# Performance work log

Measured on AMD Instinct MI355X. Metric: run time of the kernel, lower is better.

Reference implementation:

```python
import jax, jax.numpy as jnp
import numpy as np

K = 3; STRIDE = 1; PAD = 1
IN_C = 256; OUT_C = 512
M = 5; TABLE_SIZE = 16
D = K * K * IN_C  # 2304


def _P(v, m):
    # ALSH preprocessing transform: append norm powers ||v||^2, ||v||^4, ...
    n2 = jnp.sum(v * v)
    powers = jnp.stack([n2 ** (2 ** i) for i in range(m)])
    return jnp.concatenate([v, powers])


def _Q(v, m):
    # ALSH query transform: append m halves
    return jnp.concatenate([v, jnp.full((m,), 0.5, v.dtype)])


def _hash_index(a, v):
    # hf followed by fmod(table_size).abs() as in the torch module
    h = jnp.floor(jnp.dot(a, v))
    return jnp.abs(jnp.mod(h, TABLE_SIZE)).astype(jnp.int32)


def _im2col(x):
    # x: (N, C, H, W) -> (K*K*C, N*h2*w2), rows ordered (kh, kw, c) to match
    # the (out, k, k, in) kernel flattening of the original module.
    N, C, H, W = x.shape
    h2 = (H - K + 2 * PAD) // STRIDE + 1
    w2 = (W - K + 2 * PAD) // STRIDE + 1
    xp = jnp.pad(x, ((0, 0), (0, 0), (PAD, PAD), (PAD, PAD)))
    cols = []
    for i in range(K):          # small fixed loop (k*k = 9)
        for j in range(K):
            cols.append(xp[:, :, i:i + h2 * STRIDE:STRIDE, j:j + w2 * STRIDE:STRIDE])
    p = jnp.stack(cols, 0)                 # (K*K, N, C, h2, w2)
    p = p.transpose(0, 2, 1, 3, 4)         # (K*K, C, N, h2, w2)
    return p.reshape(K * K * C, N * h2 * w2), h2, w2


def setup_inputs() -> dict:
    key = jax.random.key(0)
    k1, k2, k3, k4 = jax.random.split(key, 4)
    stdv = 1.0 / np.sqrt(IN_C * K * K)
    x = jax.random.normal(k1, (16, IN_C, 56, 56), dtype=jnp.float32)
    kernels = jax.random.uniform(k2, (OUT_C, D), dtype=jnp.float32,
                                 minval=-stdv, maxval=stdv)
    bias = jax.random.uniform(k3, (1, OUT_C, 1, 1), dtype=jnp.float32,
                              minval=-stdv, maxval=stdv)
    a = jax.random.normal(k4, (D + M,), dtype=jnp.float32)
    return {"x": x, "kernels": kernels, "bias": bias, "a": a, "mode": 0}


def reference(x, kernels, bias, a, mode):
    N = x.shape[0]
    patch_matr, h2, w2 = _im2col(x)  # (D, N*h2*w2)

    # --- build ALSH table: hash index per kernel row (non-differentiable) ---
    kernel_idx = jax.lax.stop_gradient(
        jax.vmap(lambda kr: _hash_index(a, _P(kr, M)))(kernels))  # (OUT_C,)

    # --- query: max over each patch row, normalized to unit vector ---
    max_row = patch_matr.max(axis=1)                    # (D,)
    unit = max_row / jnp.linalg.norm(max_row)
    q_idx = jax.lax.stop_gradient(_hash_index(a, _Q(unit, M)))

    # --- routed subset matmul, expressed as a row mask (jit-safe) ---
    mask = (kernel_idx == q_idx)                        # (OUT_C,) bool
    count = mask.sum()
    full = kernels @ patch_matr                         # (OUT_C, N*h2*w2)
    scale = jnp.where(count > 0, count / OUT_C, 1.0).astype(full.dtype)
    out = jnp.where(count > 0,
                    jnp.where(mask[:, None], full, 0.0) / scale,
                    full)

    out = out.reshape(OUT_C, N, h2 * w2).transpose(1, 0, 2)
    out = out.reshape(N, OUT_C, h2, w2)
    return out + bias
```

## Files before the change

### kernel.cpp

```cpp
#include <hip/hip_runtime.h>
#include <math.h>

#define IN_C   256
#define OUT_C  512
#define HW     3136
#define W_     56
#define D_     2304
#define TBL    16


#define XB_OFF 2375680ULL
#define XB_ROW 1856
#define P_OFF  7483392

typedef __attribute__((ext_vector_type(8))) __bf16 bf16x8;
typedef __attribute__((ext_vector_type(4))) float f32x4;

__device__ __forceinline__ ushort f2bf(float f) {
  uint b = __float_as_uint(f);
  b = b + 0x7FFFu + ((b >> 16) & 1u);
  return (ushort)(b >> 16);
}


__global__ __launch_bounds__(256) void k_setup(const float* __restrict__ x,
                                               const float* __restrict__ kern,
                                               const float* __restrict__ a,
                                               float* __restrict__ ws) {
  __shared__ __align__(16) float smem[64 * 57];
  int bx = blockIdx.x, t = threadIdx.x;

  if (bx < 3712) {
    int c0i = bx & 3;
    int n = (bx >> 2) & 15;
    int yp = bx >> 6;
    int c0 = c0i * 64, cgbase = c0i * 2;
    ushort* xb = (ushort*)((char*)ws + XB_OFF);
    const size_t CGS = (size_t)16 * 58 * XB_ROW;
    size_t rb0 = (size_t)(n * 58 + yp) * XB_ROW;
    uint4 z4 = make_uint4(0u, 0u, 0u, 0u);

    if (yp == 0 || yp == 57) {
      for (int e = t; e < 464; e += 256) {
        int cg_l = e / 232, k = e - cg_l * 232;
        *(uint4*)&xb[rb0 + (size_t)(cgbase + cg_l) * CGS + (size_t)k * 8] = z4;
      }
      return;
    }
    if (t < 16) {
      int cg_l = t >> 3, r = t & 7;
      int wp = (r >> 2) ? 57 : 0, oct = r & 3;
      *(uint4*)&xb[rb0 + (size_t)(cgbase + cg_l) * CGS + wp * 32 + oct * 8] = z4;
    }
    int y = yp - 1;
    float* Lf = smem;
    for (int e = t; e < 3584; e += 256) {
      int ci = e / 56, w = e - ci * 56;
      Lf[ci * 57 + w] = x[(size_t)(n * 256 + c0 + ci) * 3136 + y * 56 + w];
    }
    __syncthreads();
    for (int e = t; e < 448; e += 256) {
      int w = e >> 3, cg_l = (e >> 2) & 1, oct = e & 3;
      int cb = cg_l * 32 + oct * 8;
      uint pk[4];
#pragma unroll
      for (int k = 0; k < 4; k++) {
        uint lo = f2bf(Lf[(cb + 2 * k) * 57 + w]);
        uint hi = f2bf(Lf[(cb + 2 * k + 1) * 57 + w]);
        pk[k] = lo | (hi << 16);
      }
      *(uint4*)&xb[rb0 + (size_t)(cgbase + cg_l) * CGS + (w + 1) * 32 + oct * 8] =
          make_uint4(pk[0], pk[1], pk[2], pk[3]);
    }
  } else if (bx < 4736) {
    int idx = bx - 3712;
    int c = idx & 255, part = idx >> 8;
    float m[3][3];
#pragma unroll
    for (int i = 0; i < 3; i++)
#pragma unroll
      for (int j = 0; j < 3; j++) m[i][j] = -INFINITY;
    for (int e = t; e < 4 * HW; e += 256) {
      int nl = e / HW;
      int rem = e - nl * HW;
      int r = rem / W_;
      int s = rem - r * W_;
      float v = x[(size_t)((part * 4 + nl) * IN_C + c) * HW + rem];
      bool rc[3] = { r <= 54, true, r >= 1 };
      bool sc[3] = { s <= 54, true, s >= 1 };
#pragma unroll
      for (int i = 0; i < 3; i++)
#pragma unroll
        for (int j = 0; j < 3; j++)
          if (rc[i] && sc[j]) m[i][j] = fmaxf(m[i][j], v);
    }
#pragma unroll
    for (int i = 0; i < 3; i++)
#pragma unroll
      for (int j = 0; j < 3; j++)
        for (int o = 32; o; o >>= 1)
          m[i][j] = fmaxf(m[i][j], __shfl_down(m[i][j], o, 64));
    float* red = smem;
    int lane = t & 63, wid = t >> 6;
    if (lane == 0) {
#pragma unroll
      for (int i = 0; i < 3; i++)
#pragma unroll
        for (int j = 0; j < 3; j++) red[wid * 9 + i * 3 + j] = m[i][j];
    }
    __syncthreads();
    if (t < 9) {
      float v = fmaxf(fmaxf(red[0 * 9 + t], red[1 * 9 + t]),
                      fmaxf(red[2 * 9 + t], red[3 * 9 + t]));
      ws[P_OFF + (size_t)part * 2304 + (size_t)t * IN_C + c] = v;
    }
  } else if (bx < 5248) {
    int o = bx - 4736;
    const float* kr = kern + (size_t)o * D_;
    double sd = 0, sn = 0;
    for (int d = t; d < D_; d += 256) {
      double w = (double)kr[d];
      sd += (double)a[d] * w;
      sn += w * w;
    }
    double* sh = (double*)smem;
    double* sh2 = sh + 8;
    int lane = t & 63, wid = t >> 6;
    for (int off = 32; off; off >>= 1) {
      sd += __shfl_down(sd, off, 64);
      sn += __shfl_down(sn, off, 64);
    }
    if (lane == 0) { sh[wid] = sd; sh2[wid] = sn; }
    __syncthreads();
    if (t == 0) {
      double td = 0, tn = 0;
      for (int w = 0; w < 4; w++) { td += sh[w]; tn += sh2[w]; }
      double p1 = tn, p2 = p1 * p1, p4 = p2 * p2, p8 = p4 * p4, p16 = p8 * p8;
      td += (double)a[D_] * p1 + (double)a[D_ + 1] * p2 + (double)a[D_ + 2] * p4 +
            (double)a[D_ + 3] * p8 + (double)a[D_ + 4] * p16;
      long long h = (long long)floor(td);
      ((int*)ws)[2304 + o] = (int)((h % TBL + TBL) % TBL);
    }
  } else {
    int s = bx - 5248;
    uint* Wc = (uint*)((char*)ws + 16384);
    const float* src = kern + (size_t)s * D_;
    for (int e = t; e < 1152; e += 256) {
      uint lo = f2bf(src[2 * e]);
      uint hi = f2bf(src[2 * e + 1]);
      Wc[(size_t)s * 1152 + e] = lo | (hi << 16);
    }
  }
}

__global__ __launch_bounds__(512) void k_route(const float* __restrict__ a,
                                               float* __restrict__ ws) {
  int t = threadIdx.x;
  const float* P = ws + P_OFF;
  __shared__ double sh[8], sh2[8];
  __shared__ int shq, c1, c2;
  double sd = 0.0, sq = 0.0;
  if (t < 256) {
    for (int d = t; d < D_; d += 256) {
      float v = fmaxf(fmaxf(P[d], P[2304 + d]), fmaxf(P[4608 + d], P[6912 + d]));
      if ((d >> 8) != 4) v = fmaxf(v, 0.0f);
      double dv = (double)v;
      sd += (double)a[d] * dv;
      sq += dv * dv;
    }
    for (int o = 32; o; o >>= 1) {
      sd += __shfl_down(sd, o, 64);
      sq += __shfl_down(sq, o, 64);
    }
    if ((t & 63) == 0) { sh[t >> 6] = sd; sh2[t >> 6] = sq; }
  }
  __syncthreads();
  if (t == 0) {
    double td = 0, tq = 0;
    for (int w = 0; w < 4; w++) { td += sh[w]; tq += sh2[w]; }
    double dot = td / sqrt(tq);
    dot += 0.5 * ((double)a[D_] + (double)a[D_ + 1] + (double)a[D_ + 2] +
                  (double)a[D_ + 3] + (double)a[D_ + 4]);
    long long h = (long long)floor(dot);
    int q = (int)((h % TBL + TBL) % TBL);
    ((int*)ws)[2816] = q;
    shq = q;
    c1 = 0; c2 = 0;
  }
  __syncthreads();
  int* hashk = (int*)ws + 2304;
  int* cntp = (int*)ws + 2817;
  float* scalep = ws + 2818;
  int* active = (int*)ws + 2819;
  int* inact = (int*)ws + 3331;
  int q = shq;
  bool m = (hashk[t] == q);
  if (m) active[atomicAdd(&c1, 1)] = t;
  else   inact[atomicAdd(&c2, 1)] = t;
  __syncthreads();
  int c = c1;
  if (c == 0) active[t] = t;
  if (t == 0) {
    if (c > 0) { *cntp = c; *scalep = 512.0f / (float)c; }
    else       { *cntp = 512; *scalep = 1.0f; }
  }
}

#define XSTR 40
#define XSTRIDE 40
#define ASTRIDE 104

__global__ __launch_bounds__(256, 2) void k_convx(const float* __restrict__ bias,
                                                  const float* __restrict__ ws,
                                                  float* __restrict__ out) {
  const int* iws = (const int*)ws;
  int cnt = iws[2817];
  int octile = blockIdx.y;
  int rt = blockIdx.x;
  int n = blockIdx.z;
  int t = threadIdx.x;

  {
    int base = octile * 128;
    int lo = base < cnt ? cnt : base;
    int hi = base + 128;
    if (lo < hi) {
      const int* inact = iws + 3331;
      size_t nbase = (size_t)n * OUT_C * HW;
      int nin = hi - lo;
      for (int e = t; e < nin * 56; e += 256) {
        int j = e / 56, f = e - j * 56;
        int oc = inact[lo - cnt + j];
        float bv = bias[oc];
        ((float4*)out)[(nbase + (size_t)oc * HW + rt * 224) / 4 + f] =
            make_float4(bv, bv, bv, bv);
      }
    }
    if (base >= cnt) return;
  }

  float sc = ws[2818];
  const int* active = iws + 2819;
  const char* Wcb = (const char*)ws + 16384;
  const ushort* xb = (const ushort*)((const char*)ws + XB_OFF);

  int lane = t & 63, wid = t >> 6;
  int quad = lane >> 4, l16 = lane & 15;
  int ochalf = wid & 1, pxhalf = wid >> 1;

  __shared__ __align__(16) ushort X_lds[2][348 * XSTR];

  int pbase[7];
#pragma unroll
  for (int b = 0; b < 7; b++) {
    int pxl = pxhalf * 112 + b * 16 + l16;
    int rl = pxl / 56;
    int col = pxl - rl * 56;
    pbase[b] = ((rl + 1) * 58 + (col + 1)) * XSTR;
  }

  uint woff[4];
#pragma unroll
  for (int a = 0; a < 4; a++) {
    int slot = octile * 128 + ochalf * 64 + a * 16 + l16;
    int aoc = (slot < cnt) ? active[slot] : 0;
    woff[a] = (uint)aoc * 4608u + (uint)quad * 16u;
  }

  const size_t CGS = (size_t)16 * 58 * XB_ROW;
  const ushort* xsrc = xb + (size_t)(n * 58 + rt * 4) * XB_ROW;

  f32x4 acc[4][7];
#pragma unroll
  for (int a = 0; a < 4; a++)
#pragma unroll
    for (int b = 0; b < 7; b++) acc[a][b] = (f32x4){0.f, 0.f, 0.f, 0.f};

  uint4 curA[4], nA[4];
  uint4 xh; int xhj = 0; bool xhv = false;

  {
#pragma unroll
    for (int a = 0; a < 4; a++)
      curA[a] = *(const uint4*)(Wcb + woff[a]);
    for (int j = t; j < 1392; j += 256)
      *(uint4*)&X_lds[0][(j >> 2) * XSTR + (j & 3) * 8] =
          *(const uint4*)(xsrc + (size_t)j * 8);
  }
  __syncthreads();

  for (int cc = 0; cc < 8; ++cc) {
    const int xc = cc & 1;
#pragma unroll
    for (int tap = 0; tap < 9; ++tap) {
      const int tapn = (tap + 1) % 9;
      const int ccn = cc + (tap + 1) / 9;
      const bool havenext = !(cc == 7 && tap == 8);
      if (havenext) {
        uint go = (uint)(tapn * 512) + (uint)ccn * 64u;
#pragma unroll
        for (int a = 0; a < 4; a++)
          nA[a] = *(const uint4*)(Wcb + woff[a] + go);
      }
      const bool xpf = (tap < 6) && (cc < 7) && (t < 232);
      uint4 xv; int xj = tap * 232 + t;
      if (xpf)
        xv = *(const uint4*)(xsrc + (size_t)(cc + 1) * CGS + (size_t)xj * 8);

      const int kh = tap / 3, kw = tap - kh * 3;
      const int poff = ((kh - 1) * 58 + (kw - 1)) * XSTR + quad * 8;
      __builtin_amdgcn_s_setprio(1);
#pragma unroll
      for (int b = 0; b < 7; b++) {
        union { uint4 u; bf16x8 v; } cv;
        cv.u = *(const uint4*)&X_lds[xc][pbase[b] + poff];
        bf16x8 xf = cv.v;
#pragma unroll
        for (int a = 0; a < 4; a++) {
          union { uint4 u; bf16x8 v; } av;
          av.u = curA[a];
          acc[a][b] = __builtin_amdgcn_mfma_f32_16x16x32_bf16(av.v, xf,
                                                              acc[a][b], 0, 0, 0);
        }
      }
      __builtin_amdgcn_s_setprio(0);

      if (xhv)
        *(uint4*)&X_lds[xc ^ 1][(xhj >> 2) * XSTR + (xhj & 3) * 8] = xh;
      xh = xv; xhj = xj; xhv = xpf;
      if (havenext) {
#pragma unroll
        for (int a = 0; a < 4; a++) curA[a] = nA[a];
      }
    }
    __syncthreads();
  }

  size_t nbase = (size_t)n * OUT_C * HW;
#pragma unroll
  for (int a = 0; a < 4; a++) {
#pragma unroll
    for (int r = 0; r < 4; r++) {
      int slot = octile * 128 + ochalf * 64 + a * 16 + quad * 4 + r;
      if (slot < cnt) {
        int oc = active[slot];
        float bv = bias[oc];
        size_t obase = nbase + (size_t)oc * HW + rt * 224 + pxhalf * 112 + l16;
#pragma unroll
        for (int b = 0; b < 7; b++)
          out[obase + b * 16] = acc[a][b][r] * sc + bv;
      }
    }
  }
}


__global__ __launch_bounds__(256) void k_chanmax(const float* __restrict__ x,
                                                 float* __restrict__ ws) {
  int c = blockIdx.x, t = threadIdx.x;
  float m[3][3];
#pragma unroll
  for (int i = 0; i < 3; i++)
#pragma unroll
    for (int j = 0; j < 3; j++) m[i][j] = -INFINITY;
  for (int e = t; e < 16 * HW; e += 256) {
    int n = e / HW;
    int rem = e - n * HW;
    int r = rem / W_;
    int s = rem - r * W_;
    float v = x[(size_t)(n * IN_C + c) * HW + rem];
    bool rc[3] = { r <= 54, true, r >= 1 };
    bool sc[3] = { s <= 54, true, s >= 1 };
#pragma unroll
    for (int i = 0; i < 3; i++)
#pragma unroll
      for (int j = 0; j < 3; j++)
        if (rc[i] && sc[j]) m[i][j] = fmaxf(m[i][j], v);
  }
#pragma unroll
  for (int i = 0; i < 3; i++)
#pragma unroll
    for (int j = 0; j < 3; j++)
      for (int o = 32; o; o >>= 1)
        m[i][j] = fmaxf(m[i][j], __shfl_down(m[i][j], o, 64));
  __shared__ float red[4][9];
  int lane = t & 63, wid = t >> 6;
  if (lane == 0) {
#pragma unroll
    for (int i = 0; i < 3; i++)
#pragma unroll
      for (int j = 0; j < 3; j++) red[wid][i * 3 + j] = m[i][j];
  }
  __syncthreads();
  if (t < 9) {
    float v = fmaxf(fmaxf(red[0][t], red[1][t]), fmaxf(red[2][t], red[3][t]));
    int i = t / 3, j = t - i * 3;
    if (i != 1 || j != 1) v = fmaxf(v, 0.0f);
    ws[(size_t)t * IN_C + c] = v;
  }
}

__global__ __launch_bounds__(256) void k_qhash(const float* __restrict__ a,
                                               float* __restrict__ ws) {
  const float* max_row = ws;
  int t = threadIdx.x;
  double sd = 0.0, sq = 0.0;
  for (int d = t; d < D_; d += 256) {
    double v = (double)max_row[d];
    sd += (double)a[d] * v;
    sq += v * v;
  }
  __shared__ double sh[8], sh2[8];
  int lane = t & 63, wid = t >> 6;
  for (int o = 32; o; o >>= 1) {
    sd += __shfl_down(sd, o, 64);
    sq += __shfl_down(sq, o, 64);
  }
  if (lane == 0) { sh[wid] = sd; sh2[wid] = sq; }
  __syncthreads();
  if (t == 0) {
    double td = 0, tq = 0;
    for (int w = 0; w < 4; w++) { td += sh[w]; tq += sh2[w]; }
    double dot = td / sqrt(tq);
    dot += 0.5 * ((double)a[D_] + (double)a[D_ + 1] + (double)a[D_ + 2] +
                  (double)a[D_ + 3] + (double)a[D_ + 4]);
    long long h = (long long)floor(dot);
    ((int*)ws)[2816] = (int)((h % TBL + TBL) % TBL);
  }
}

__global__ __launch_bounds__(256) void k_khash(const float* __restrict__ kern,
                                               const float* __restrict__ a,
                                               float* __restrict__ ws) {
  int o = blockIdx.x, t = threadIdx.x;
  const float* kr = kern + (size_t)o * D_;
  double sd = 0, sn = 0;
  for (int d = t; d < D_; d += 256) {
    double w = (double)kr[d];
    sd += (double)a[d] * w;
    sn += w * w;
  }
  __shared__ double sh[8], sh2[8];
  int lane = t & 63, wid = t >> 6;
  for (int off = 32; off; off >>= 1) {
    sd += __shfl_down(sd, off, 64);
    sn += __shfl_down(sn, off, 64);
  }
  if (lane == 0) { sh[wid] = sd; sh2[wid] = sn; }
  __syncthreads();
  if (t == 0) {
    double td = 0, tn = 0;
    for (int w = 0; w < 4; w++) { td += sh[w]; tn += sh2[w]; }
    double p1 = tn, p2 = p1 * p1, p4 = p2 * p2, p8 = p4 * p4, p16 = p8 * p8;
    td += (double)a[D_] * p1 + (double)a[D_ + 1] * p2 + (double)a[D_ + 2] * p4 +
          (double)a[D_ + 3] * p8 + (double)a[D_ + 4] * p16;
    long long h = (long long)floor(td);
    ((int*)ws)[2304 + o] = (int)((h % TBL + TBL) % TBL);
  }
}

__global__ __launch_bounds__(512) void k_select(float* __restrict__ ws) {
  int t = threadIdx.x;
  int* hashk = (int*)ws + 2304;
  int* qidx = (int*)ws + 2816;
  int* cntp = (int*)ws + 2817;
  float* scalep = ws + 2818;
  int* active = (int*)ws + 2819;
  int* flags = (int*)ws + 3331;
  __shared__ int cnt;
  if (t == 0) cnt = 0;
  active[t] = 0;
  __syncthreads();
  int q = *qidx;
  bool m = (hashk[t] == q);
  if (m) {
    int p = atomicAdd(&cnt, 1);
    active[p] = t;
  }
  __syncthreads();
  int c = cnt;
  flags[t] = (c == 0) ? 1 : (m ? 1 : 0);
  if (c == 0) active[t] = t;
  if (t == 0) {
    if (c > 0) { *cntp = c; *scalep = 512.0f / (float)c; }
    else       { *cntp = 512; *scalep = 1.0f; }
  }
}

__global__ __launch_bounds__(256) void k_prep(const float* __restrict__ kern,
                                              float* __restrict__ ws) {
  const int* iws = (const int*)ws;
  int cnt = iws[2817];
  const int* active = iws + 2819;
  ushort* Wc = (ushort*)((char*)ws + 16384);
  int s = blockIdx.x, t = threadIdx.x;
  if (s < cnt) {
    int oc = active[s];
    const float* src = kern + (size_t)oc * D_;
    for (int e = t; e < D_; e += 256) Wc[(size_t)s * D_ + e] = f2bf(src[e]);
  } else {
    for (int e = t; e < D_; e += 256) Wc[(size_t)s * D_ + e] = 0;
  }
}

__global__ __launch_bounds__(256) void k_biasfill(const float* __restrict__ bias,
                                                  const float* __restrict__ ws,
                                                  float* __restrict__ out) {
  const int* flags = (const int*)ws + 3331;
  const int total4 = 16 * OUT_C * HW / 4;
  int stride = gridDim.x * blockDim.x;
  for (int i = blockIdx.x * blockDim.x + threadIdx.x; i < total4; i += stride) {
    int o = (i / 784) & (OUT_C - 1);
    if (!flags[o]) {
      float b = bias[o];
      ((float4*)out)[i] = make_float4(b, b, b, b);
    }
  }
}

__global__ __launch_bounds__(256, 2) void k_conv(const float* __restrict__ x,
                                                 const float* __restrict__ bias,
                                                 const float* __restrict__ ws,
                                                 float* __restrict__ out) {
  const int* iws = (const int*)ws;
  int cnt = iws[2817];
  int octile = blockIdx.y;
  if (octile * 128 >= cnt) return;
  float sc = ws[2818];
  const int* active = iws + 2819;
  const ushort* Wc = (const ushort*)((const char*)ws + 16384);
  int rt = blockIdx.x;
  int n = blockIdx.z;
  int t = threadIdx.x;
  int lane = t & 63, wid = t >> 6;
  int quad = lane >> 4, l16 = lane & 15;
  int ochalf = wid & 1, pxhalf = wid >> 1;
  __shared__ __align__(16) ushort X_lds[348 * XSTRIDE];
  __shared__ __align__(16) ushort A_lds[128 * ASTRIDE];
  const float* xin = x + (size_t)n * IN_C * HW;
  int pbase[7];
#pragma unroll
  for (int b = 0; b < 7; b++) {
    int pxl = pxhalf * 112 + b * 16 + l16;
    int rl = pxl / 56;
    int col = pxl - rl * 56;
    pbase[b] = ((rl + 1) * 58 + (col + 1)) * XSTRIDE;
  }
  f32x4 acc[4][7];
#pragma unroll
  for (int a = 0; a < 4; a++)
#pragma unroll
    for (int b = 0; b < 7; b++) acc[a][b] = (f32x4){0.f, 0.f, 0.f, 0.f};
  for (int cc = 0; cc < 8; ++cc) {
    int c0 = cc * 32;
    __syncthreads();
    for (int e = t; e < 1392; e += 256) {
      int q = e / 348;
      int p = e - q * 348;
      int rl = p / 58;
      int cp = p - rl * 58;
      int y = rt * 4 - 1 + rl;
      int xx = cp - 1;
      float vv[8];
      if ((unsigned)y < 56u && (unsigned)xx < 56u) {
        const float* src = xin + (size_t)(c0 + q * 8) * HW + y * W_ + xx;
#pragma unroll
        for (int k = 0; k < 8; k++) vv[k] = src[(size_t)k * HW];
      } else {
#pragma unroll
        for (int k = 0; k < 8; k++) vv[k] = 0.f;
      }
      uint4 pk;
      pk.x = (uint)f2bf(vv[0]) | ((uint)f2bf(vv[1]) << 16);
      pk.y = (uint)f2bf(vv[2]) | ((uint)f2bf(vv[3]) << 16);
      pk.z = (uint)f2bf(vv[4]) | ((uint)f2bf(vv[5]) << 16);
      pk.w = (uint)f2bf(vv[6]) | ((uint)f2bf(vv[7]) << 16);
      *(uint4*)&X_lds[p * XSTRIDE + q * 8] = pk;
    }
    for (int kh = 0; kh < 3; ++kh) {
      __syncthreads();
      for (int e = t; e < 1536; e += 256) {
        int oc = e / 12;
        int seg = e - oc * 12;
        int tl = seg >> 2, q = seg & 3;
        uint4 v = *(const uint4*)(Wc + (size_t)(octile * 128 + oc) * D_ +
                                  (kh * 3 + tl) * IN_C + c0 + q * 8);
        *(uint4*)&A_lds[oc * ASTRIDE + tl * 32 + q * 8] = v;
      }
      __syncthreads();
      int di = kh - 1;
#pragma unroll
      for (int djj = 0; djj < 3; ++djj) {
        int poff = (di * 58 + (djj - 1)) * XSTRIDE + quad * 8;
        bf16x8 bfr[7];
#pragma unroll
        for (int b = 0; b < 7; b++) {
          union { uint4 u; bf16x8 v; } cv;
          cv.u = *(const uint4*)&X_lds[pbase[b] + poff];
          bfr[b] = cv.v;
        }
#pragma unroll
        for (int a = 0; a < 4; a++) {
          union { uint4 u; bf16x8 v; } cv;
          cv.u = *(const uint4*)&A_lds[(ochalf * 64 + a * 16 + l16) * ASTRIDE +
                                       djj * 32 + quad * 8];
          bf16x8 af = cv.v;
#pragma unroll
          for (int b = 0; b < 7; b++)
            acc[a][b] = __builtin_amdgcn_mfma_f32_16x16x32_bf16(af, bfr[b],
                                                                acc[a][b], 0, 0, 0);
        }
      }
    }
  }
  size_t nbase = (size_t)n * OUT_C * HW;
#pragma unroll
  for (int a = 0; a < 4; a++) {
#pragma unroll
    for (int r = 0; r < 4; r++) {
      int slot = octile * 128 + ochalf * 64 + a * 16 + quad * 4 + r;
      if (slot < cnt) {
        int oc = active[slot];
        float bv = bias[oc];
        size_t obase = nbase + (size_t)oc * HW + rt * 224 + pxhalf * 112 + l16;
#pragma unroll
        for (int b = 0; b < 7; b++)
          out[obase + b * 16] = acc[a][b][r] * sc + bv;
      }
    }
  }
}

extern "C" void kernel_launch(void* const* d_in, const int* in_sizes, int n_in,
                              void* d_out, int out_size, void* d_ws, size_t ws_size,
                              hipStream_t stream) {
  const float* x    = (const float*)d_in[0];
  const float* kern = (const float*)d_in[1];
  const float* bias = (const float*)d_in[2];
  const float* a    = (const float*)d_in[3];
  float* out = (float*)d_out;
  float* ws  = (float*)d_ws;

  const size_t need = 29933568ULL + 4 * 2304 * 4;

  if (ws_size >= need) {
    k_setup<<<dim3(5760), dim3(256), 0, stream>>>(x, kern, a, ws);
    k_route<<<dim3(1), dim3(512), 0, stream>>>(a, ws);
    k_convx<<<dim3(14, 4, 16), dim3(256), 0, stream>>>(bias, ws, out);
  } else {
    k_chanmax<<<dim3(IN_C), dim3(256), 0, stream>>>(x, ws);
    k_qhash<<<dim3(1), dim3(256), 0, stream>>>(a, ws);
    k_khash<<<dim3(OUT_C), dim3(256), 0, stream>>>(kern, a, ws);
    k_select<<<dim3(1), dim3(512), 0, stream>>>(ws);
    k_prep<<<dim3(OUT_C), dim3(256), 0, stream>>>(kern, ws);
    k_biasfill<<<dim3(4096), dim3(256), 0, stream>>>(bias, ws, out);
    k_conv<<<dim3(14, 4, 16), dim3(256), 0, stream>>>(x, bias, ws, out);
  }
}
```

Baseline: 340.1 us.

## Enlarge conv tile to 128 channels by 448 pixels and stage weights in LDS

The implicit-GEMM conv block now covers 8 image rows (448 pixels) instead of 4, and each wave computes all 128 output channels over 112 pixels with 8x7 accumulators. Weights are staged through a double-buffered LDS tile shared by all waves instead of being loaded per wave into registers. This halves the grid and raises reuse of both the activation halo and the weights. The cost is doubled accumulator registers (occupancy hint lowered to 1), a larger LDS footprint, and a block barrier after every tap instead of once per channel group.

```diff
diff --git a/kernel.cpp b/kernel.cpp
--- a/kernel.cpp
+++ b/kernel.cpp
@@ -210,7 +210,7 @@
 #define XSTRIDE 40
 #define ASTRIDE 104
 
-__global__ __launch_bounds__(256, 2) void k_convx(const float* __restrict__ bias,
+__global__ __launch_bounds__(256, 1) void k_convx(const float* __restrict__ bias,
                                                   const float* __restrict__ ws,
                                                   float* __restrict__ out) {
   const int* iws = (const int*)ws;
@@ -228,11 +228,11 @@
       const int* inact = iws + 3331;
       size_t nbase = (size_t)n * OUT_C * HW;
       int nin = hi - lo;
-      for (int e = t; e < nin * 56; e += 256) {
-        int j = e / 56, f = e - j * 56;
+      for (int e = t; e < nin * 112; e += 256) {
+        int j = e / 112, f = e - j * 112;
         int oc = inact[lo - cnt + j];
         float bv = bias[oc];
-        ((float4*)out)[(nbase + (size_t)oc * HW + rt * 224) / 4 + f] =
+        ((float4*)out)[(nbase + (size_t)oc * HW) / 4 + rt * 112 + f] =
             make_float4(bv, bv, bv, bv);
       }
     }
@@ -246,44 +246,46 @@
 
   int lane = t & 63, wid = t >> 6;
   int quad = lane >> 4, l16 = lane & 15;
-  int ochalf = wid & 1, pxhalf = wid >> 1;
-
-  __shared__ __align__(16) ushort X_lds[2][348 * XSTR];
+
+  __shared__ __align__(16) ushort X_lds[2][580 * XSTR];
+  __shared__ __align__(16) ushort A_lds[2][128 * XSTR];
 
   int pbase[7];
 #pragma unroll
   for (int b = 0; b < 7; b++) {
-    int pxl = pxhalf * 112 + b * 16 + l16;
+    int pxl = wid * 112 + b * 16 + l16;
     int rl = pxl / 56;
     int col = pxl - rl * 56;
     pbase[b] = ((rl + 1) * 58 + (col + 1)) * XSTR;
   }
 
-  uint woff[4];
-#pragma unroll
-  for (int a = 0; a < 4; a++) {
-    int slot = octile * 128 + ochalf * 64 + a * 16 + l16;
-    int aoc = (slot < cnt) ? active[slot] : 0;
-    woff[a] = (uint)aoc * 4608u + (uint)quad * 16u;
-  }
+  int r0 = t >> 2;
+  int slot0 = octile * 128 + r0;
+  int slot1 = slot0 + 64;
+  int aoc0 = (slot0 < cnt) ? active[slot0] : 0;
+  int aoc1 = (slot1 < cnt) ? active[slot1] : 0;
+  const char* Wr0 = Wcb + (size_t)aoc0 * 4608 + (t & 3) * 16;
+  const char* Wr1 = Wcb + (size_t)aoc1 * 4608 + (t & 3) * 16;
+  int aoff0 = r0 * XSTR + (t & 3) * 8;
+  int aoff1 = (r0 + 64) * XSTR + (t & 3) * 8;
 
   const size_t CGS = (size_t)16 * 58 * XB_ROW;
-  const ushort* xsrc = xb + (size_t)(n * 58 + rt * 4) * XB_ROW;
-
-  f32x4 acc[4][7];
-#pragma unroll
-  for (int a = 0; a < 4; a++)
+  const ushort* xsrc = xb + (size_t)(n * 58 + rt * 8) * XB_ROW;
+
+  f32x4 acc[8][7];
+#pragma unroll
+  for (int a = 0; a < 8; a++)
 #pragma unroll
     for (int b = 0; b < 7; b++) acc[a][b] = (f32x4){0.f, 0.f, 0.f, 0.f};
 
-  uint4 curA[4], nA[4];
-  uint4 xh; int xhj = 0; bool xhv = false;
+  uint4 xh0 = {}, xh1 = {};
 
   {
-#pragma unroll
-    for (int a = 0; a < 4; a++)
-      curA[a] = *(const uint4*)(Wcb + woff[a]);
-    for (int j = t; j < 1392; j += 256)
+    uint4 a0 = *(const uint4*)Wr0;
+    uint4 a1 = *(const uint4*)Wr1;
+    *(uint4*)&A_lds[0][aoff0] = a0;
+    *(uint4*)&A_lds[0][aoff1] = a1;
+    for (int j = t; j < 2320; j += 256)
       *(uint4*)&X_lds[0][(j >> 2) * XSTR + (j & 3) * 8] =
           *(const uint4*)(xsrc + (size_t)j * 8);
   }
@@ -293,59 +295,75 @@
     const int xc = cc & 1;
 #pragma unroll
     for (int tap = 0; tap < 9; ++tap) {
+      const int cur = (cc + tap) & 1;
       const int tapn = (tap + 1) % 9;
       const int ccn = cc + (tap + 1) / 9;
       const bool havenext = !(cc == 7 && tap == 8);
+      uint4 na0, na1;
       if (havenext) {
-        uint go = (uint)(tapn * 512) + (uint)ccn * 64u;
-#pragma unroll
-        for (int a = 0; a < 4; a++)
-          nA[a] = *(const uint4*)(Wcb + woff[a] + go);
-      }
-      const bool xpf = (tap < 6) && (cc < 7) && (t < 232);
-      uint4 xv; int xj = tap * 232 + t;
-      if (xpf)
-        xv = *(const uint4*)(xsrc + (size_t)(cc + 1) * CGS + (size_t)xj * 8);
+        int off = tapn * 512 + ccn * 64;
+        na0 = *(const uint4*)(Wr0 + off);
+        na1 = *(const uint4*)(Wr1 + off);
+      }
+      const bool xi = (tap < 8) && (cc < 7);
+      uint4 xv0, xv1;
+      if (xi) {
+        int xj = tap * 290 + t;
+        xv0 = *(const uint4*)(xsrc + (size_t)(cc + 1) * CGS + (size_t)xj * 8);
+        if (t < 34)
+          xv1 = *(const uint4*)(xsrc + (size_t)(cc + 1) * CGS +
+                                (size_t)(xj + 256) * 8);
+      }
 
       const int kh = tap / 3, kw = tap - kh * 3;
       const int poff = ((kh - 1) * 58 + (kw - 1)) * XSTR + quad * 8;
-      __builtin_amdgcn_s_setprio(1);
+      bf16x8 xf[7];
 #pragma unroll
       for (int b = 0; b < 7; b++) {
         union { uint4 u; bf16x8 v; } cv;
         cv.u = *(const uint4*)&X_lds[xc][pbase[b] + poff];
-        bf16x8 xf = cv.v;
-#pragma unroll
-        for (int a = 0; a < 4; a++) {
-          union { uint4 u; bf16x8 v; } av;
-          av.u = curA[a];
-          acc[a][b] = __builtin_amdgcn_mfma_f32_16x16x32_bf16(av.v, xf,
+        xf[b] = cv.v;
+      }
+      __builtin_amdgcn_s_setprio(1);
+#pragma unroll
+      for (int a = 0; a < 8; a++) {
+        union { uint4 u; bf16x8 v; } av;
+        av.u = *(const uint4*)&A_lds[cur][(a * 16 + l16) * XSTR + quad * 8];
+        bf16x8 af = av.v;
+#pragma unroll
+        for (int b = 0; b < 7; b++)
+          acc[a][b] = __builtin_amdgcn_mfma_f32_16x16x32_bf16(af, xf[b],
                                                               acc[a][b], 0, 0, 0);
+      }
+      __builtin_amdgcn_s_setprio(0);
+
+      if (havenext) {
+        *(uint4*)&A_lds[cur ^ 1][aoff0] = na0;
+        *(uint4*)&A_lds[cur ^ 1][aoff1] = na1;
+      }
+      if (tap >= 1 && cc < 7) {
+        int hj = (tap - 1) * 290 + t;
+        *(uint4*)&X_lds[xc ^ 1][(hj >> 2) * XSTR + (hj & 3) * 8] = xh0;
+        if (t < 34) {
+          int hj2 = hj + 256;
+          *(uint4*)&X_lds[xc ^ 1][(hj2 >> 2) * XSTR + (hj2 & 3) * 8] = xh1;
         }
       }
-      __builtin_amdgcn_s_setprio(0);
-
-      if (xhv)
-        *(uint4*)&X_lds[xc ^ 1][(xhj >> 2) * XSTR + (xhj & 3) * 8] = xh;
-      xh = xv; xhj = xj; xhv = xpf;
-      if (havenext) {
-#pragma unroll
-        for (int a = 0; a < 4; a++) curA[a] = nA[a];
-      }
-    }
-    __syncthreads();
+      xh0 = xv0; xh1 = xv1;
+      __syncthreads();
+    }
   }
 
   size_t nbase = (size_t)n * OUT_C * HW;
 #pragma unroll
-  for (int a = 0; a < 4; a++) {
+  for (int a = 0; a < 8; a++) {
 #pragma unroll
     for (int r = 0; r < 4; r++) {
-      int slot = octile * 128 + ochalf * 64 + a * 16 + quad * 4 + r;
+      int slot = octile * 128 + a * 16 + quad * 4 + r;
       if (slot < cnt) {
         int oc = active[slot];
         float bv = bias[oc];
-        size_t obase = nbase + (size_t)oc * HW + rt * 224 + pxhalf * 112 + l16;
+        size_t obase = nbase + (size_t)oc * HW + rt * 448 + wid * 112 + l16;
 #pragma unroll
         for (int b = 0; b < 7; b++)
           out[obase + b * 16] = acc[a][b][r] * sc + bv;
@@ -646,7 +664,7 @@
   if (ws_size >= need) {
     k_setup<<<dim3(5760), dim3(256), 0, stream>>>(x, kern, a, ws);
     k_route<<<dim3(1), dim3(512), 0, stream>>>(a, ws);
-    k_convx<<<dim3(14, 4, 16), dim3(256), 0, stream>>>(bias, ws, out);
+    k_convx<<<dim3(7, 4, 16), dim3(256), 0, stream>>>(bias, ws, out);
   } else {
     k_chanmax<<<dim3(IN_C), dim3(256), 0, stream>>>(x, ws);
     k_qhash<<<dim3(1), dim3(256), 0, stream>>>(a, ws);
```

After: 323.0 us. -5.0%, faster.
